# Performance work log

Measured on AMD Instinct MI355X. Metric: run time of the kernel, lower is better.

The kernel has to match this reference:

```python
import jax, jax.numpy as jnp
import numpy as np

NUM_HEADS = 16
HIDDEN = 2048
HEAD_DIM = HIDDEN // NUM_HEADS


def setup_inputs() -> dict:
    key = jax.random.key(0)
    ks = jax.random.split(key, 9)
    B, S, D = 2, 2048, HIDDEN
    s = 0.02
    return {
        "hidden_states": jax.random.normal(ks[0], (B, S, D), jnp.float32),
        "attention_mask": jnp.ones((B, S), jnp.float32),
        "Wq": jax.random.normal(ks[1], (D, D), jnp.float32) * s,
        "bq": jnp.zeros((D,), jnp.float32),
        "Wk": jax.random.normal(ks[2], (D, D), jnp.float32) * s,
        "bk": jnp.zeros((D,), jnp.float32),
        "Wv": jax.random.normal(ks[3], (D, D), jnp.float32) * s,
        "bv": jnp.zeros((D,), jnp.float32),
        "Wo": jax.random.normal(ks[4], (D, D), jnp.float32) * s,
        "bo": jnp.zeros((D,), jnp.float32),
    }


def _split_heads(x, B, S):
    # [B, S, D] -> [B, H, S, hd]
    return x.reshape(B, S, NUM_HEADS, HEAD_DIM).transpose(0, 2, 1, 3)


def reference(hidden_states, attention_mask, Wq, bq, Wk, bk, Wv, bv, Wo, bo):
    B, S, D = hidden_states.shape
    scale = HEAD_DIM ** -0.5
    # Projections (torch Linear: x @ W.T + b); q scaled as in source
    q = (jnp.einsum('bsd,ed->bse', hidden_states, Wq) + bq) * scale
    k = jnp.einsum('bsd,ed->bse', hidden_states, Wk) + bk
    v = jnp.einsum('bsd,ed->bse', hidden_states, Wv) + bv
    q = _split_heads(q, B, S)
    k = _split_heads(k, B, S)
    v = _split_heads(v, B, S)
    # scores: [B, H, S, S]
    scores = jnp.einsum('bhqd,bhkd->bhqk', q, k)
    # 2D mask path: [B, S] -> additive mask broadcast over heads/query
    add_mask = (1.0 - attention_mask)[:, None, None, :] * jnp.finfo(scores.dtype).min
    scores = scores + add_mask
    attn = jax.nn.softmax(scores, axis=-1)
    out = jnp.einsum('bhqk,bhkd->bhqd', attn, v)
    out = out.transpose(0, 2, 1, 3).reshape(B, S, D)
    out = jnp.einsum('bsd,ed->bse', out, Wo) + bo
    return out
```

## Files before the change

### kernel.cpp

```cpp
#include <hip/hip_runtime.h>

typedef unsigned short u16;
typedef unsigned int   u32;
typedef __attribute__((ext_vector_type(8))) short short8;
typedef __attribute__((ext_vector_type(4))) float f32x4;

#define DEVI static __device__ __forceinline__

DEVI u16 f2bf(float f) {
  u32 u = __float_as_uint(f);
  u32 r = (u + 0x7FFFu + ((u >> 16) & 1u)) >> 16;
  return (u16)r;
}

DEVI void gload_lds16(const void* g, void* l) {
  __builtin_amdgcn_global_load_lds(
      (const __attribute__((address_space(1))) void*)g,
      (__attribute__((address_space(3))) void*)l, 16, 0, 0);
}

__global__ void __launch_bounds__(256) cvt_kernel(const float4* __restrict__ src,
                                                  uint4* __restrict__ dst, int n8) {
  int i = blockIdx.x * 256 + threadIdx.x;
  if (i >= n8) return;
  float4 a = src[2 * i], b = src[2 * i + 1];
  uint4 o;
  o.x = (u32)f2bf(a.x) | ((u32)f2bf(a.y) << 16);
  o.y = (u32)f2bf(a.z) | ((u32)f2bf(a.w) << 16);
  o.z = (u32)f2bf(b.x) | ((u32)f2bf(b.y) << 16);
  o.w = (u32)f2bf(b.z) | ((u32)f2bf(b.w) << 16);
  dst[i] = o;
}

__global__ void __launch_bounds__(256) cvt4_kernel(
    const float4* __restrict__ s0, const float4* __restrict__ s1,
    const float4* __restrict__ s2, const float4* __restrict__ s3,
    uint4* __restrict__ d0, uint4* __restrict__ d1,
    uint4* __restrict__ d2, uint4* __restrict__ d3, int n8) {
  int i = blockIdx.x * 256 + threadIdx.x;
  if (i >= n8) return;
  int seg = blockIdx.y;
  const float4* s = (seg == 0) ? s0 : (seg == 1) ? s1 : (seg == 2) ? s2 : s3;
  uint4* d = (seg == 0) ? d0 : (seg == 1) ? d1 : (seg == 2) ? d2 : d3;
  float4 a = s[2 * i], b = s[2 * i + 1];
  uint4 o;
  o.x = (u32)f2bf(a.x) | ((u32)f2bf(a.y) << 16);
  o.y = (u32)f2bf(a.z) | ((u32)f2bf(a.w) << 16);
  o.z = (u32)f2bf(b.x) | ((u32)f2bf(b.y) << 16);
  o.w = (u32)f2bf(b.z) | ((u32)f2bf(b.w) << 16);
  d[i] = o;
}

template <int MODE>
__global__ void __launch_bounds__(256) gemm_bt(
    const u16* __restrict__ A, const u16* __restrict__ Bw, void* __restrict__ Cp,
    const float* __restrict__ bias0, const float* __restrict__ bias1,
    const float* __restrict__ bias2, int ldc) {
  constexpr int K = 2048;
  __shared__ __align__(16) u16 As[128 * 32];
  __shared__ __align__(16) u16 Bs[128 * 32];
  const int tid = threadIdx.x, w = tid >> 6, l = tid & 63;
  const int wm = w >> 1, wn = w & 1;
  const int bm = blockIdx.x, bn = blockIdx.y;
  const char* Ab = (const char*)(A + (size_t)bm * 128 * K);
  const char* Bb = (const char*)(Bw + (size_t)bn * 128 * K);
  f32x4 acc[4][4] = {};
  for (int kt = 0; kt < K / 32; ++kt) {
#pragma unroll
    for (int q = 0; q < 2; ++q) {
      int byteoff = q * 4096 + w * 1024 + l * 16;
      int row = byteoff >> 6, colb = byteoff & 63;
      gload_lds16(Ab + (size_t)row * (K * 2) + kt * 64 + colb,
                  (char*)As + q * 4096 + w * 1024);
      gload_lds16(Bb + (size_t)row * (K * 2) + kt * 64 + colb,
                  (char*)Bs + q * 4096 + w * 1024);
    }
    __syncthreads();
    short8 af[4], bf[4];
#pragma unroll
    for (int mi = 0; mi < 4; ++mi)
      af[mi] = *(const short8*)((const char*)As + (wm * 64 + mi * 16 + (l & 15)) * 64 + (l >> 4) * 16);
#pragma unroll
    for (int ni = 0; ni < 4; ++ni)
      bf[ni] = *(const short8*)((const char*)Bs + (wn * 64 + ni * 16 + (l & 15)) * 64 + (l >> 4) * 16);
#pragma unroll
    for (int mi = 0; mi < 4; ++mi)
#pragma unroll
      for (int ni = 0; ni < 4; ++ni)
        acc[mi][ni] = __builtin_amdgcn_mfma_f32_16x16x32_bf16(af[mi], bf[ni], acc[mi][ni], 0, 0, 0);
    __syncthreads();
  }
#pragma unroll
  for (int mi = 0; mi < 4; ++mi) {
    int grow = bm * 128 + wm * 64 + mi * 16 + ((l >> 4) << 2);
#pragma unroll
    for (int ni = 0; ni < 4; ++ni) {
      int gcol = bn * 128 + wn * 64 + ni * 16 + (l & 15);
#pragma unroll
      for (int j = 0; j < 4; ++j) {
        float v = acc[mi][ni][j];
        if (MODE == 0) {
          int seg = gcol >> 11;
          const float* bp = (seg == 0) ? bias0 : (seg == 1 ? bias1 : bias2);
          v += bp[gcol & 2047];
          if (seg == 0) v *= 0.08838834764831845f;
          ((u16*)Cp)[(size_t)(grow + j) * ldc + gcol] = f2bf(v);
        } else {
          ((float*)Cp)[(size_t)(grow + j) * ldc + gcol] = v + bias0[gcol];
        }
      }
    }
  }
}

__global__ void __launch_bounds__(256, 2) attn_kernel(const u16* __restrict__ qkv,
                                                      const float* __restrict__ amask,
                                                      u16* __restrict__ ctx) {
  __shared__ __align__(16) char KtB[64 * 256];
  __shared__ __align__(16) char VtB[128 * 128];
  __shared__ __align__(16) char PbB[4][2][2048];
  const int tid = threadIdx.x, w = tid >> 6, l = tid & 63;
  const int l15 = l & 15, l4 = l >> 4;
  const int qt = blockIdx.x & 15, h = (blockIdx.x >> 4) & 15, b = (int)(blockIdx.x >> 8);
  const int ld = 6144;
  const int swq = (l15 & 7) << 4;
  short8 qf[2][4];
#pragma unroll
  for (int qg = 0; qg < 2; ++qg) {
    const u16* qp = qkv + (size_t)(b * 2048 + qt * 128 + w * 32 + qg * 16 + l15) * ld + h * 128;
#pragma unroll
    for (int dc = 0; dc < 4; ++dc) qf[qg][dc] = *(const short8*)(qp + dc * 32 + l4 * 8);
  }
  f32x4 o_[2][8] = {};
  float m_[2] = {-INFINITY, -INFINITY}, s_[2] = {0.f, 0.f};
  const u16* kbase = qkv + (size_t)b * 2048 * ld + 2048 + h * 128;
  const u16* vbase = qkv + (size_t)b * 2048 * ld + 4096 + h * 128;
  const float* mbase = amask + b * 2048;
  const int kr = tid >> 2, c0 = (tid & 3) * 32;
  const int kb = (tid & 15) * 4, dvb = (tid >> 4) * 8;
  for (int t = 0; t < 32; ++t) {
    const int k0 = t * 64;
    __syncthreads();
    {
      const u16* kg = kbase + (size_t)(k0 + kr) * ld + c0;
      char* drow = KtB + kr * 256;
      const int sw = (kr & 7) << 4;
#pragma unroll
      for (int u = 0; u < 4; ++u)
        *(uint4*)(drow + ((c0 * 2 + u * 16) ^ sw)) = *(const uint4*)(kg + u * 8);
      uint4 vr[4];
#pragma unroll
      for (int r = 0; r < 4; ++r)
        vr[r] = *(const uint4*)(vbase + (size_t)(k0 + kb + r) * ld + dvb);
#pragma unroll
      for (int dvi = 0; dvi < 8; ++dvi) {
        int dv = dvb + dvi;
        u32 lo = (u32)((const u16*)&vr[0])[dvi] | ((u32)((const u16*)&vr[1])[dvi] << 16);
        u32 hi = (u32)((const u16*)&vr[2])[dvi] | ((u32)((const u16*)&vr[3])[dvi] << 16);
        uint2 pk; pk.x = lo; pk.y = hi;
        *(uint2*)(VtB + dv * 128 + ((kb * 2) ^ ((dv & 7) << 4))) = pk;
      }
    }
    __syncthreads();
    float4 amv[4];
#pragma unroll
    for (int kc = 0; kc < 4; ++kc) {
      float4 mv = *(const float4*)(mbase + k0 + kc * 16 + l4 * 4);
      amv[kc].x = (1.0f - mv.x) * -3.402823466e38f;
      amv[kc].y = (1.0f - mv.y) * -3.402823466e38f;
      amv[kc].z = (1.0f - mv.z) * -3.402823466e38f;
      amv[kc].w = (1.0f - mv.w) * -3.402823466e38f;
    }
    f32x4 sA[2][4];
#pragma unroll
    for (int kc = 0; kc < 4; ++kc) {
      const int krow = kc * 16 + l15;
      const char* krp = KtB + krow * 256;
      const int sw = (krow & 7) << 4;
      short8 kf[4];
#pragma unroll
      for (int dc = 0; dc < 4; ++dc)
        kf[dc] = *(const short8*)(krp + ((dc * 64 + l4 * 16) ^ sw));
#pragma unroll
      for (int qg = 0; qg < 2; ++qg) {
        f32x4 tacc = {0.f, 0.f, 0.f, 0.f};
#pragma unroll
        for (int dc = 0; dc < 4; ++dc)
          tacc = __builtin_amdgcn_mfma_f32_16x16x32_bf16(kf[dc], qf[qg][dc], tacc, 0, 0, 0);
        sA[qg][kc] = tacc;
      }
    }
    float fct[2];
#pragma unroll
    for (int qg = 0; qg < 2; ++qg) {
      float pm = -INFINITY;
#pragma unroll
      for (int kc = 0; kc < 4; ++kc) {
        sA[qg][kc][0] += amv[kc].x; sA[qg][kc][1] += amv[kc].y;
        sA[qg][kc][2] += amv[kc].z; sA[qg][kc][3] += amv[kc].w;
#pragma unroll
        for (int j = 0; j < 4; ++j) pm = fmaxf(pm, sA[qg][kc][j]);
      }
      pm = fmaxf(pm, __shfl_xor(pm, 16));
      pm = fmaxf(pm, __shfl_xor(pm, 32));
      float mn = fmaxf(m_[qg], pm);
      fct[qg] = __expf(m_[qg] - mn);
      m_[qg] = mn;
      float rs = 0.f;
#pragma unroll
      for (int kc = 0; kc < 4; ++kc) {
#pragma unroll
        for (int j = 0; j < 4; ++j) {
          float p = __expf(sA[qg][kc][j] - mn);
          rs += p;
          sA[qg][kc][j] = p;
        }
        u32 lo = (u32)f2bf(sA[qg][kc][0]) | ((u32)f2bf(sA[qg][kc][1]) << 16);
        u32 hi = (u32)f2bf(sA[qg][kc][2]) | ((u32)f2bf(sA[qg][kc][3]) << 16);
        uint2 pk; pk.x = lo; pk.y = hi;
        *(uint2*)(PbB[w][qg] + l15 * 128 + ((kc * 32 + l4 * 8) ^ swq)) = pk;
      }
      rs += __shfl_xor(rs, 16);
      rs += __shfl_xor(rs, 32);
      s_[qg] = s_[qg] * fct[qg] + rs;
    }
#pragma unroll
    for (int qg = 0; qg < 2; ++qg) {
      float fq[4];
#pragma unroll
      for (int j = 0; j < 4; ++j) fq[j] = __shfl(fct[qg], l4 * 4 + j);
#pragma unroll
      for (int dvc = 0; dvc < 8; ++dvc)
#pragma unroll
        for (int j = 0; j < 4; ++j) o_[qg][dvc][j] *= fq[j];
    }
    short8 pa[2][2];
#pragma unroll
    for (int qg = 0; qg < 2; ++qg)
#pragma unroll
      for (int kh = 0; kh < 2; ++kh)
        pa[qg][kh] = *(const short8*)(PbB[w][qg] + l15 * 128 + ((kh * 64 + l4 * 16) ^ swq));
#pragma unroll
    for (int dvc = 0; dvc < 8; ++dvc) {
      const int dv = dvc * 16 + l15;
      const char* vrp = VtB + dv * 128;
      const int swv = (dv & 7) << 4;
#pragma unroll
      for (int kh = 0; kh < 2; ++kh) {
        short8 vf = *(const short8*)(vrp + ((kh * 64 + l4 * 16) ^ swv));
#pragma unroll
        for (int qg = 0; qg < 2; ++qg)
          o_[qg][dvc] = __builtin_amdgcn_mfma_f32_16x16x32_bf16(pa[qg][kh], vf, o_[qg][dvc], 0, 0, 0);
      }
    }
  }
#pragma unroll
  for (int qg = 0; qg < 2; ++qg) {
    float inv = 1.0f / s_[qg];
    float iq[4];
#pragma unroll
    for (int j = 0; j < 4; ++j) iq[j] = __shfl(inv, l4 * 4 + j);
    u16* crow = ctx + (size_t)(b * 2048 + qt * 128 + w * 32 + qg * 16 + l4 * 4) * 2048 + h * 128;
#pragma unroll
    for (int dvc = 0; dvc < 8; ++dvc)
#pragma unroll
      for (int j = 0; j < 4; ++j)
        crow[(size_t)j * 2048 + dvc * 16 + l15] = f2bf(o_[qg][dvc][j] * iq[j]);
  }
}

extern "C" void kernel_launch(void* const* d_in, const int* in_sizes, int n_in,
                              void* d_out, int out_size, void* d_ws, size_t ws_size,
                              hipStream_t stream) {
  const float* hs    = (const float*)d_in[0];
  const float* amask = (const float*)d_in[1];
  const float* Wq    = (const float*)d_in[2];
  const float* bq    = (const float*)d_in[3];
  const float* Wk    = (const float*)d_in[4];
  const float* bk    = (const float*)d_in[5];
  const float* Wv    = (const float*)d_in[6];
  const float* bv    = (const float*)d_in[7];
  const float* Wo    = (const float*)d_in[8];
  const float* bo    = (const float*)d_in[9];
  float* out = (float*)d_out;

  char* ws = (char*)d_ws;
  u16* hiddenB = (u16*)ws;
  u16* wcatB   = (u16*)(ws + 16777216ull);
  u16* woB     = (u16*)(ws + 16777216ull + 25165824ull);
  u16* qkvB    = (u16*)(ws + 16777216ull + 25165824ull + 8388608ull);
  u16* ctxB    = (u16*)(ws + 16777216ull + 25165824ull + 8388608ull + 50331648ull);

  cvt_kernel<<<4096, 256, 0, stream>>>((const float4*)hs, (uint4*)hiddenB, 1048576);
  cvt4_kernel<<<dim3(2048, 4), 256, 0, stream>>>(
      (const float4*)Wq, (const float4*)Wk, (const float4*)Wv, (const float4*)Wo,
      (uint4*)wcatB, (uint4*)(wcatB + 2048 * 2048), (uint4*)(wcatB + 2 * 2048 * 2048),
      (uint4*)woB, 524288);

  gemm_bt<0><<<dim3(32, 48), 256, 0, stream>>>(hiddenB, wcatB, qkvB, bq, bk, bv, 6144);
  attn_kernel<<<512, 256, 0, stream>>>(qkvB, amask, ctxB);
  gemm_bt<1><<<dim3(32, 16), 256, 0, stream>>>(ctxB, woB, out, bo, nullptr, nullptr, 2048);
}
```

Before: 429.1 us.

## Swizzle GEMM blocks, DMA K tiles to LDS, lazy rescale, MFMA priority

Remaps the GEMM block index with an XCD-style swizzle so neighbouring tiles share cache. In attention, K tiles are now loaded with global_load_lds direct-to-LDS instead of through registers. The online softmax skips the max update and accumulator rescaling unless the running max grows by more than 8 (lazy rescale). s_setprio raises wave priority around the MFMA sections. The lazy threshold keeps exponentials bounded but changes the numerics slightly.

```diff
diff --git a/kernel.cpp b/kernel.cpp
--- a/kernel.cpp
+++ b/kernel.cpp
@@ -61,7 +61,10 @@
   __shared__ __align__(16) u16 Bs[128 * 32];
   const int tid = threadIdx.x, w = tid >> 6, l = tid & 63;
   const int wm = w >> 1, wn = w & 1;
-  const int bm = blockIdx.x, bn = blockIdx.y;
+  const int nbm = gridDim.x, nwg = gridDim.x * gridDim.y;
+  const int lid = blockIdx.y * gridDim.x + blockIdx.x;
+  const int swz = (lid & 7) * (nwg >> 3) + (lid >> 3);
+  const int bm = swz % nbm, bn = swz / nbm;
   const char* Ab = (const char*)(A + (size_t)bm * 128 * K);
   const char* Bb = (const char*)(Bw + (size_t)bn * 128 * K);
   f32x4 acc[4][4] = {};
@@ -136,18 +139,19 @@
   const u16* kbase = qkv + (size_t)b * 2048 * ld + 2048 + h * 128;
   const u16* vbase = qkv + (size_t)b * 2048 * ld + 4096 + h * 128;
   const float* mbase = amask + b * 2048;
-  const int kr = tid >> 2, c0 = (tid & 3) * 32;
   const int kb = (tid & 15) * 4, dvb = (tid >> 4) * 8;
   for (int t = 0; t < 32; ++t) {
     const int k0 = t * 64;
     __syncthreads();
     {
-      const u16* kg = kbase + (size_t)(k0 + kr) * ld + c0;
-      char* drow = KtB + kr * 256;
-      const int sw = (kr & 7) << 4;
-#pragma unroll
-      for (int u = 0; u < 4; ++u)
-        *(uint4*)(drow + ((c0 * 2 + u * 16) ^ sw)) = *(const uint4*)(kg + u * 8);
+      const char* kt_src = (const char*)kbase + (size_t)(k0 + w * 16) * 12288;
+#pragma unroll
+      for (int u = 0; u < 4; ++u) {
+        const int ru = u * 4 + l4;
+        const int colb = (l15 * 16) ^ ((ru & 7) << 4);
+        gload_lds16(kt_src + (size_t)ru * 12288 + colb,
+                    (char*)KtB + (w * 4 + u) * 1024);
+      }
       uint4 vr[4];
 #pragma unroll
       for (int r = 0; r < 4; ++r)
@@ -172,6 +176,7 @@
       amv[kc].w = (1.0f - mv.w) * -3.402823466e38f;
     }
     f32x4 sA[2][4];
+    __builtin_amdgcn_s_setprio(1);
 #pragma unroll
     for (int kc = 0; kc < 4; ++kc) {
       const int krow = kc * 16 + l15;
@@ -190,7 +195,7 @@
         sA[qg][kc] = tacc;
       }
     }
-    float fct[2];
+    __builtin_amdgcn_s_setprio(0);
 #pragma unroll
     for (int qg = 0; qg < 2; ++qg) {
       float pm = -INFINITY;
@@ -203,15 +208,25 @@
       }
       pm = fmaxf(pm, __shfl_xor(pm, 16));
       pm = fmaxf(pm, __shfl_xor(pm, 32));
-      float mn = fmaxf(m_[qg], pm);
-      fct[qg] = __expf(m_[qg] - mn);
-      m_[qg] = mn;
+      if (!__all(pm - m_[qg] <= 8.0f)) {
+        float mn = fmaxf(m_[qg], pm);
+        float fct = __expf(m_[qg] - mn);
+        m_[qg] = mn;
+        s_[qg] *= fct;
+        float fq[4];
+#pragma unroll
+        for (int j = 0; j < 4; ++j) fq[j] = __shfl(fct, l4 * 4 + j);
+#pragma unroll
+        for (int dvc = 0; dvc < 8; ++dvc)
+#pragma unroll
+          for (int j = 0; j < 4; ++j) o_[qg][dvc][j] *= fq[j];
+      }
       float rs = 0.f;
 #pragma unroll
       for (int kc = 0; kc < 4; ++kc) {
 #pragma unroll
         for (int j = 0; j < 4; ++j) {
-          float p = __expf(sA[qg][kc][j] - mn);
+          float p = __expf(sA[qg][kc][j] - m_[qg]);
           rs += p;
           sA[qg][kc][j] = p;
         }
@@ -222,17 +237,7 @@
       }
       rs += __shfl_xor(rs, 16);
       rs += __shfl_xor(rs, 32);
-      s_[qg] = s_[qg] * fct[qg] + rs;
-    }
-#pragma unroll
-    for (int qg = 0; qg < 2; ++qg) {
-      float fq[4];
-#pragma unroll
-      for (int j = 0; j < 4; ++j) fq[j] = __shfl(fct[qg], l4 * 4 + j);
-#pragma unroll
-      for (int dvc = 0; dvc < 8; ++dvc)
-#pragma unroll
-        for (int j = 0; j < 4; ++j) o_[qg][dvc][j] *= fq[j];
+      s_[qg] += rs;
     }
     short8 pa[2][2];
 #pragma unroll
@@ -240,6 +245,7 @@
 #pragma unroll
       for (int kh = 0; kh < 2; ++kh)
         pa[qg][kh] = *(const short8*)(PbB[w][qg] + l15 * 128 + ((kh * 64 + l4 * 16) ^ swq));
+    __builtin_amdgcn_s_setprio(1);
 #pragma unroll
     for (int dvc = 0; dvc < 8; ++dvc) {
       const int dv = dvc * 16 + l15;
@@ -253,6 +259,7 @@
           o_[qg][dvc] = __builtin_amdgcn_mfma_f32_16x16x32_bf16(pa[qg][kh], vf, o_[qg][dvc], 0, 0, 0);
       }
     }
+    __builtin_amdgcn_s_setprio(0);
   }
 #pragma unroll
   for (int qg = 0; qg < 2; ++qg) {
```

Measured after the change: 444.0 us. 1.03x slower.
